# Kernel optimization log

Measured on AMD Instinct MI355X. Metric: run time of the kernel, lower is better.

## Reference

```python
import jax, jax.numpy as jnp
import numpy as np

HEADS = 12
DIM = 768
DH = DIM // HEADS


def setup_inputs() -> dict:
    key = jax.random.key(0)
    k1, k2 = jax.random.split(key)
    z = jax.random.normal(k1, (4, 2048, DIM), dtype=jnp.float32)
    # nn.Linear(dim, 3*dim, bias=False): weight shape [3*dim, dim], y = z @ W.T
    W_qkv = jax.random.normal(k2, (3 * DIM, DIM), dtype=jnp.float32) * (1.0 / np.sqrt(DIM))
    return {"z": z, "W_qkv": W_qkv}


def reference(z, W_qkv):
    b, n, d = z.shape
    qkv = jnp.einsum('bnd,ed->bne', z, W_qkv)  # [b, n, 3*dim]
    # last dim layout is (headNum, m, Dh) per the einops pattern '(headNum m Dh)'
    qkv = qkv.reshape(b, n, HEADS, 3, DH)
    q = jnp.transpose(qkv[:, :, :, 0, :], (0, 2, 1, 3))  # [b, h, n, Dh]
    k = jnp.transpose(qkv[:, :, :, 1, :], (0, 2, 1, 3))
    v = jnp.transpose(qkv[:, :, :, 2, :], (0, 2, 1, 3))
    scores = jnp.einsum('bhqd,bhkd->bhqk', q, k) / np.sqrt(DH).astype(np.float32)
    A = jax.nn.softmax(scores, axis=-1)  # full [b, h, n, n] matrix, as in source
    out = jnp.einsum('bhqk,bhkd->bhqd', A, v)  # [b, h, n, Dh]
    return jnp.transpose(out, (0, 2, 1, 3)).reshape(b, n, d)
```

## Files before the change

### kernel.cpp

```cpp
#include <hip/hip_runtime.h>
#include <hip/hip_bf16.h>
#include <stdint.h>


typedef __attribute__((ext_vector_type(8))) short bf8_t;
typedef __attribute__((ext_vector_type(4))) float f4_t;

__device__ __forceinline__ unsigned short f2bf(float f) {
  union { float f; unsigned u; } x; x.f = f;
  return (unsigned short)((x.u + 0x7fffu + ((x.u >> 16) & 1u)) >> 16);
}
__device__ __forceinline__ unsigned cvt_pk_bf16(float lo, float hi) {
  unsigned r;
  asm("v_cvt_pk_bf16_f32 %0, %1, %2" : "=v"(r) : "v"(lo), "v"(hi));
  return r;
}
__device__ __forceinline__ void gload_lds16(const void* g, void* l) {
  __builtin_amdgcn_global_load_lds(
      (const __attribute__((address_space(1))) void*)g,
      (__attribute__((address_space(3))) void*)l, 16, 0, 0);
}

__global__ __launch_bounds__(256) void cvt_kernel(
    const float* __restrict__ Z, const float* __restrict__ W,
    unsigned short* __restrict__ Zb)
{
  const int idx = blockIdx.x * 256 + threadIdx.x;
  const float* src;
  unsigned short* dst;
  int c;
  if (idx < 786432) { src = Z; dst = Zb; c = idx; }
  else              { src = W; dst = Zb + 6291456; c = idx - 786432; }
  const float4 a0 = *(const float4*)(src + (size_t)c * 8);
  const float4 a1 = *(const float4*)(src + (size_t)c * 8 + 4);
  uint4 pk = { cvt_pk_bf16(a0.x, a0.y), cvt_pk_bf16(a0.z, a0.w),
               cvt_pk_bf16(a1.x, a1.y), cvt_pk_bf16(a1.z, a1.w) };
  *(uint4*)(dst + (size_t)c * 8) = pk;
}

__global__ __launch_bounds__(256, 3) void qkv_gemm_kernel(
    const unsigned short* __restrict__ Zb, const unsigned short* __restrict__ Wb,
    unsigned short* __restrict__ qb, unsigned short* __restrict__ kb,
    unsigned short* __restrict__ vt)
{
  __shared__ __align__(16) unsigned short As[128 * 64];
  __shared__ __align__(16) unsigned short Bs[128 * 64];

  const int tid = threadIdx.x;
  const int w    = tid >> 6;
  const int lane = tid & 63;
  const int g    = lane >> 4;
  const int l15  = lane & 15;
  const int bid0 = blockIdx.y * 18 + blockIdx.x;
  const int bid  = (bid0 & 7) * 144 + (bid0 >> 3);
  const int m0 = (bid / 18) * 128;
  const int n0 = (bid % 18) * 128;
  const int wr = w >> 1, wc = w & 1;

  const int arow = w * 32 + (lane >> 3);
  const int achk = ((lane & 7) ^ (lane >> 3)) * 8;
  const unsigned short* za = Zb + (size_t)(m0 + arow) * 768 + achk;
  const unsigned short* wa = Wb + (size_t)(n0 + arow) * 768 + achk;
  unsigned short* const lza = As + w * 32 * 64;
  unsigned short* const lwa = Bs + w * 32 * 64;

  const f4_t zf = {0.f, 0.f, 0.f, 0.f};
  f4_t acc[4][4];
#pragma unroll
  for (int m = 0; m < 4; ++m)
#pragma unroll
    for (int n = 0; n < 4; ++n) acc[m][n] = zf;

  for (int ks = 0; ks < 12; ++ks) {
    __syncthreads();
#pragma unroll
    for (int r = 0; r < 4; ++r) {
      gload_lds16(za + r * 8 * 768, lza + r * 512);
      gload_lds16(wa + r * 8 * 768, lwa + r * 512);
    }
    za += 64; wa += 64;
    __syncthreads();

#pragma unroll
    for (int s = 0; s < 2; ++s) {
      bf8_t af[4], bfr[4];
#pragma unroll
      for (int m = 0; m < 4; ++m) {
        const int row = wr * 64 + m * 16 + l15;
        af[m] = *(const bf8_t*)(As + row * 64 + (((s * 4 + g) ^ (row & 7)) * 8));
      }
#pragma unroll
      for (int n = 0; n < 4; ++n) {
        const int row = wc * 64 + n * 16 + l15;
        bfr[n] = *(const bf8_t*)(Bs + row * 64 + (((s * 4 + g) ^ (row & 7)) * 8));
      }
      __builtin_amdgcn_s_setprio(1);
#pragma unroll
      for (int m = 0; m < 4; ++m)
#pragma unroll
        for (int n = 0; n < 4; ++n)
          acc[m][n] = __builtin_amdgcn_mfma_f32_16x16x32_bf16(af[m], bfr[n], acc[m][n], 0, 0, 0);
      __builtin_amdgcn_s_setprio(0);
    }
  }

  const float QSCALE = 0.18033688011112042f;
#pragma unroll
  for (int m = 0; m < 4; ++m) {
    const int gi  = m0 + wr * 64 + m * 16 + g * 4;
    const int b   = gi >> 11;
    const int tok = gi & 2047;
#pragma unroll
    for (int n = 0; n < 4; ++n) {
      const int e0  = n0 + wc * 64 + n * 16;
      const int h   = e0 / 192;
      const int rem = e0 - h * 192;
      const int mm  = rem >> 6;
      const int dh  = (rem & 63) + l15;
      if (mm == 2) {
        uint2 pk = { cvt_pk_bf16(acc[m][n][0], acc[m][n][1]),
                     cvt_pk_bf16(acc[m][n][2], acc[m][n][3]) };
        const int pos = ((tok >> 5) & 1) * 32 + ((tok >> 2) & 3) * 8
                      + ((tok >> 4) & 1) * 4;
        const size_t vaddr = ((size_t)(b * 12 + h) * 32 + (tok >> 6)) * 4096
                           + dh * 64 + pos;
        *(uint2*)(vt + vaddr) = pk;
      } else {
        unsigned short* buf = mm ? kb : qb;
        const float sc = mm ? 1.0f : QSCALE;
        const size_t base = ((size_t)((b * 12 + h) * 2048 + tok)) * 64 + dh;
#pragma unroll
        for (int j = 0; j < 4; ++j)
          buf[base + (size_t)j * 64] = f2bf(acc[m][n][j] * sc);
      }
    }
  }
}

__global__ __launch_bounds__(256, 3) void attn_kernel(
    const unsigned short* __restrict__ qb, const unsigned short* __restrict__ kb,
    const unsigned short* __restrict__ vt, float* __restrict__ out)
{
  __shared__ __align__(16) unsigned short Ks[2][64 * 64];
  __shared__ __align__(16) unsigned short Vs[2][64 * 64];

  const int bid = blockIdx.x;
  const int nb  = (bid & 7) * 96 + (bid >> 3);
  const int bh  = nb >> 4;
  const int qt  = nb & 15;
  const int tid = threadIdx.x;
  const int w    = tid >> 6;
  const int lane = tid & 63;
  const int g    = lane >> 4;
  const int l15  = lane & 15;

  const unsigned short* Qh  = qb + (size_t)bh * 2048 * 64;
  const unsigned short* Kh  = kb + (size_t)bh * 2048 * 64;
  const unsigned short* VTh = vt + (size_t)bh * 32 * 4096;

  const int qbase = qt * 128 + w * 32;

  bf8_t qfr[2][2];
#pragma unroll
  for (int qq = 0; qq < 2; ++qq)
#pragma unroll
    for (int s = 0; s < 2; ++s)
      qfr[qq][s] = *(const bf8_t*)(Qh + (size_t)(qbase + qq * 16 + l15) * 64 + s * 32 + g * 8);

  const int xk   = l15 & 7;
  const int offA = l15 * 64 + ((g) ^ xk) * 8;
  const int offB = l15 * 64 + ((4 + g) ^ xk) * 8;

  const size_t dmaoff = (size_t)(w * 16 + (lane >> 3)) * 64
                      + ((lane & 7) ^ (lane >> 3)) * 8;
  const unsigned short* ksrc = Kh + dmaoff;
  const unsigned short* vsrc = VTh + dmaoff;
  const int ldsoff = w * 16 * 64;

  gload_lds16(ksrc,                 &Ks[0][ldsoff]);
  gload_lds16(ksrc + 8 * 64,        &Ks[0][ldsoff + 8 * 64]);
  gload_lds16(vsrc,                 &Vs[0][ldsoff]);
  gload_lds16(vsrc + 8 * 64,        &Vs[0][ldsoff + 8 * 64]);
  gload_lds16(ksrc + 4096,          &Ks[1][ldsoff]);
  gload_lds16(ksrc + 4096 + 8 * 64, &Ks[1][ldsoff + 8 * 64]);
  gload_lds16(vsrc + 4096,          &Vs[1][ldsoff]);
  gload_lds16(vsrc + 4096 + 8 * 64, &Vs[1][ldsoff + 8 * 64]);
  __syncthreads();

  const unsigned short* kdma = ksrc + 2 * 4096;
  const unsigned short* vdma = vsrc + 2 * 4096;

  const f4_t m16 = {-16.f, -16.f, -16.f, -16.f};
  const f4_t zf  = {0.f, 0.f, 0.f, 0.f};
  f4_t accO[2][4];
  float lsumP[2] = {0.f, 0.f};
#pragma unroll
  for (int qq = 0; qq < 2; ++qq)
#pragma unroll
    for (int nf = 0; nf < 4; ++nf) accO[qq][nf] = zf;

  for (int t = 0; t < 32; ++t) {
    const int cur = t & 1;
    const unsigned short* pK = &Ks[cur][0];
    const unsigned short* pV = &Vs[cur][0];

    bf8_t ka[4][2];
#pragma unroll
    for (int kf = 0; kf < 4; ++kf) {
      ka[kf][0] = *(const bf8_t*)(pK + offA + kf * 1024);
      ka[kf][1] = *(const bf8_t*)(pK + offB + kf * 1024);
    }
    bf8_t vfr[2][4];
#pragma unroll
    for (int nf = 0; nf < 4; ++nf) {
      vfr[0][nf] = *(const bf8_t*)(pV + offA + nf * 1024);
      vfr[1][nf] = *(const bf8_t*)(pV + offB + nf * 1024);
    }

    __syncthreads();

    if (t < 30) {
      gload_lds16(kdma,          &Ks[cur][ldsoff]);
      gload_lds16(kdma + 8 * 64, &Ks[cur][ldsoff + 8 * 64]);
      gload_lds16(vdma,          &Vs[cur][ldsoff]);
      gload_lds16(vdma + 8 * 64, &Vs[cur][ldsoff + 8 * 64]);
      kdma += 4096; vdma += 4096;
    }

    f4_t accS0[4], accS1[4];
    __builtin_amdgcn_s_setprio(1);
#pragma unroll
    for (int kf = 0; kf < 4; ++kf) {
      f4_t a = __builtin_amdgcn_mfma_f32_16x16x32_bf16(ka[kf][0], qfr[0][0], m16, 0, 0, 0);
      accS0[kf] = __builtin_amdgcn_mfma_f32_16x16x32_bf16(ka[kf][1], qfr[0][1], a, 0, 0, 0);
    }
#pragma unroll
    for (int kf = 0; kf < 4; ++kf) {
      f4_t a = __builtin_amdgcn_mfma_f32_16x16x32_bf16(ka[kf][0], qfr[1][0], m16, 0, 0, 0);
      accS1[kf] = __builtin_amdgcn_mfma_f32_16x16x32_bf16(ka[kf][1], qfr[1][1], a, 0, 0, 0);
    }
    __builtin_amdgcn_s_setprio(0);

#pragma unroll
    for (int qq = 0; qq < 2; ++qq) {
      const f4_t* accS = qq ? accS1 : accS0;
      union { bf8_t v[2]; unsigned uw[8]; } P8;
      float ps = 0.f;
#pragma unroll
      for (int kf = 0; kf < 4; ++kf) {
        const float p0 = __builtin_amdgcn_exp2f(accS[kf][0]);
        const float p1 = __builtin_amdgcn_exp2f(accS[kf][1]);
        const float p2 = __builtin_amdgcn_exp2f(accS[kf][2]);
        const float p3 = __builtin_amdgcn_exp2f(accS[kf][3]);
        ps += (p0 + p1) + (p2 + p3);
        P8.uw[kf * 2]     = cvt_pk_bf16(p0, p1);
        P8.uw[kf * 2 + 1] = cvt_pk_bf16(p2, p3);
      }
      lsumP[qq] += ps;

      __builtin_amdgcn_s_setprio(1);
#pragma unroll
      for (int kk = 0; kk < 2; ++kk)
#pragma unroll
        for (int nf = 0; nf < 4; ++nf)
          accO[qq][nf] = __builtin_amdgcn_mfma_f32_16x16x32_bf16(P8.v[kk], vfr[kk][nf], accO[qq][nf], 0, 0, 0);
      __builtin_amdgcn_s_setprio(0);
    }
  }

  const int b = bh / 12, h = bh - (bh / 12) * 12;
#pragma unroll
  for (int qq = 0; qq < 2; ++qq) {
    float ls = lsumP[qq];
    ls += __shfl_xor(ls, 16);
    ls += __shfl_xor(ls, 32);
    const float rl = 1.0f / ls;
    f4_t lv;
#pragma unroll
    for (int j = 0; j < 4; ++j) lv[j] = __shfl(rl, g * 4 + j);
#pragma unroll
    for (int nf = 0; nf < 4; ++nf) {
#pragma unroll
      for (int j = 0; j < 4; ++j) {
        const int qrow = qbase + qq * 16 + g * 4 + j;
        out[((size_t)(b * 2048 + qrow)) * 768 + h * 64 + nf * 16 + l15] = accO[qq][nf][j] * lv[j];
      }
    }
  }
}

extern "C" void kernel_launch(void* const* d_in, const int* in_sizes, int n_in,
                              void* d_out, int out_size, void* d_ws, size_t ws_size,
                              hipStream_t stream) {
  (void)in_sizes; (void)n_in; (void)out_size; (void)ws_size;
  const float* Z = (const float*)d_in[0];
  const float* W = (const float*)d_in[1];
  float* out = (float*)d_out;

  unsigned short* qb = (unsigned short*)d_ws;
  unsigned short* kb = qb + (size_t)48 * 2048 * 64;
  unsigned short* vt = kb + (size_t)48 * 2048 * 64;

  unsigned short* Zb = (unsigned short*)d_out;
  unsigned short* Wb = Zb + (size_t)8192 * 768;

  cvt_kernel<<<dim3(3936), 256, 0, stream>>>(Z, W, Zb);
  qkv_gemm_kernel<<<dim3(18, 64), 256, 0, stream>>>(Zb, Wb, qb, kb, vt);
  attn_kernel<<<dim3(768), 256, 0, stream>>>(qb, kb, vt, out);
}
```

Before: 105.2 us.

## Use two waves per attention block, each handling 64 query rows

The attention kernel now runs with 128 threads (two waves) per block instead of four, and each wave processes 64 query rows (four 16-row groups) instead of 32. Each wave reuses the K and V fragments it loaded from LDS across more MFMAs, and each thread issues twice as many DMA loads. The cost is more accumulator registers per thread and fewer waves per workgroup to hide latency. Launch bounds change to (128,2), which may reduce occupancy.

```diff
diff --git a/kernel.cpp b/kernel.cpp
--- a/kernel.cpp
+++ b/kernel.cpp
@@ -137,7 +137,7 @@
   }
 }
 
-__global__ __launch_bounds__(256, 3) void attn_kernel(
+__global__ __launch_bounds__(128, 2) void attn_kernel(
     const unsigned short* __restrict__ qb, const unsigned short* __restrict__ kb,
     const unsigned short* __restrict__ vt, float* __restrict__ out)
 {
@@ -158,11 +158,11 @@
   const unsigned short* Kh  = kb + (size_t)bh * 2048 * 64;
   const unsigned short* VTh = vt + (size_t)bh * 32 * 4096;
 
-  const int qbase = qt * 128 + w * 32;
-
-  bf8_t qfr[2][2];
-#pragma unroll
-  for (int qq = 0; qq < 2; ++qq)
+  const int qbase = qt * 128 + w * 64;
+
+  bf8_t qfr[4][2];
+#pragma unroll
+  for (int qq = 0; qq < 4; ++qq)
 #pragma unroll
     for (int s = 0; s < 2; ++s)
       qfr[qq][s] = *(const bf8_t*)(Qh + (size_t)(qbase + qq * 16 + l15) * 64 + s * 32 + g * 8);
@@ -171,20 +171,19 @@
   const int offA = l15 * 64 + ((g) ^ xk) * 8;
   const int offB = l15 * 64 + ((4 + g) ^ xk) * 8;
 
-  const size_t dmaoff = (size_t)(w * 16 + (lane >> 3)) * 64
+  const size_t dmaoff = (size_t)(w * 32 + (lane >> 3)) * 64
                       + ((lane & 7) ^ (lane >> 3)) * 8;
   const unsigned short* ksrc = Kh + dmaoff;
   const unsigned short* vsrc = VTh + dmaoff;
-  const int ldsoff = w * 16 * 64;
-
-  gload_lds16(ksrc,                 &Ks[0][ldsoff]);
-  gload_lds16(ksrc + 8 * 64,        &Ks[0][ldsoff + 8 * 64]);
-  gload_lds16(vsrc,                 &Vs[0][ldsoff]);
-  gload_lds16(vsrc + 8 * 64,        &Vs[0][ldsoff + 8 * 64]);
-  gload_lds16(ksrc + 4096,          &Ks[1][ldsoff]);
-  gload_lds16(ksrc + 4096 + 8 * 64, &Ks[1][ldsoff + 8 * 64]);
-  gload_lds16(vsrc + 4096,          &Vs[1][ldsoff]);
-  gload_lds16(vsrc + 4096 + 8 * 64, &Vs[1][ldsoff + 8 * 64]);
+  const int ldsoff = w * 32 * 64;
+
+#pragma unroll
+  for (int r = 0; r < 4; ++r) {
+    gload_lds16(ksrc + r * 8 * 64,        &Ks[0][ldsoff + r * 512]);
+    gload_lds16(vsrc + r * 8 * 64,        &Vs[0][ldsoff + r * 512]);
+    gload_lds16(ksrc + 4096 + r * 8 * 64, &Ks[1][ldsoff + r * 512]);
+    gload_lds16(vsrc + 4096 + r * 8 * 64, &Vs[1][ldsoff + r * 512]);
+  }
   __syncthreads();
 
   const unsigned short* kdma = ksrc + 2 * 4096;
@@ -192,10 +191,10 @@
 
   const f4_t m16 = {-16.f, -16.f, -16.f, -16.f};
   const f4_t zf  = {0.f, 0.f, 0.f, 0.f};
-  f4_t accO[2][4];
-  float lsumP[2] = {0.f, 0.f};
-#pragma unroll
-  for (int qq = 0; qq < 2; ++qq)
+  f4_t accO[4][4];
+  float lsumP[4] = {0.f, 0.f, 0.f, 0.f};
+#pragma unroll
+  for (int qq = 0; qq < 4; ++qq)
 #pragma unroll
     for (int nf = 0; nf < 4; ++nf) accO[qq][nf] = zf;
 
@@ -220,57 +219,62 @@
     __syncthreads();
 
     if (t < 30) {
-      gload_lds16(kdma,          &Ks[cur][ldsoff]);
-      gload_lds16(kdma + 8 * 64, &Ks[cur][ldsoff + 8 * 64]);
-      gload_lds16(vdma,          &Vs[cur][ldsoff]);
-      gload_lds16(vdma + 8 * 64, &Vs[cur][ldsoff + 8 * 64]);
+#pragma unroll
+      for (int r = 0; r < 4; ++r) {
+        gload_lds16(kdma + r * 8 * 64, &Ks[cur][ldsoff + r * 512]);
+        gload_lds16(vdma + r * 8 * 64, &Vs[cur][ldsoff + r * 512]);
+      }
       kdma += 4096; vdma += 4096;
     }
 
-    f4_t accS0[4], accS1[4];
-    __builtin_amdgcn_s_setprio(1);
-#pragma unroll
-    for (int kf = 0; kf < 4; ++kf) {
-      f4_t a = __builtin_amdgcn_mfma_f32_16x16x32_bf16(ka[kf][0], qfr[0][0], m16, 0, 0, 0);
-      accS0[kf] = __builtin_amdgcn_mfma_f32_16x16x32_bf16(ka[kf][1], qfr[0][1], a, 0, 0, 0);
-    }
-#pragma unroll
-    for (int kf = 0; kf < 4; ++kf) {
-      f4_t a = __builtin_amdgcn_mfma_f32_16x16x32_bf16(ka[kf][0], qfr[1][0], m16, 0, 0, 0);
-      accS1[kf] = __builtin_amdgcn_mfma_f32_16x16x32_bf16(ka[kf][1], qfr[1][1], a, 0, 0, 0);
-    }
-    __builtin_amdgcn_s_setprio(0);
-
-#pragma unroll
-    for (int qq = 0; qq < 2; ++qq) {
-      const f4_t* accS = qq ? accS1 : accS0;
-      union { bf8_t v[2]; unsigned uw[8]; } P8;
-      float ps = 0.f;
+#pragma unroll
+    for (int qp = 0; qp < 2; ++qp) {
+      f4_t accSa[4], accSb[4];
+      __builtin_amdgcn_s_setprio(1);
 #pragma unroll
       for (int kf = 0; kf < 4; ++kf) {
-        const float p0 = __builtin_amdgcn_exp2f(accS[kf][0]);
-        const float p1 = __builtin_amdgcn_exp2f(accS[kf][1]);
-        const float p2 = __builtin_amdgcn_exp2f(accS[kf][2]);
-        const float p3 = __builtin_amdgcn_exp2f(accS[kf][3]);
-        ps += (p0 + p1) + (p2 + p3);
-        P8.uw[kf * 2]     = cvt_pk_bf16(p0, p1);
-        P8.uw[kf * 2 + 1] = cvt_pk_bf16(p2, p3);
-      }
-      lsumP[qq] += ps;
-
-      __builtin_amdgcn_s_setprio(1);
-#pragma unroll
-      for (int kk = 0; kk < 2; ++kk)
-#pragma unroll
-        for (int nf = 0; nf < 4; ++nf)
-          accO[qq][nf] = __builtin_amdgcn_mfma_f32_16x16x32_bf16(P8.v[kk], vfr[kk][nf], accO[qq][nf], 0, 0, 0);
+        f4_t a = __builtin_amdgcn_mfma_f32_16x16x32_bf16(ka[kf][0], qfr[qp * 2][0], m16, 0, 0, 0);
+        accSa[kf] = __builtin_amdgcn_mfma_f32_16x16x32_bf16(ka[kf][1], qfr[qp * 2][1], a, 0, 0, 0);
+      }
+#pragma unroll
+      for (int kf = 0; kf < 4; ++kf) {
+        f4_t a = __builtin_amdgcn_mfma_f32_16x16x32_bf16(ka[kf][0], qfr[qp * 2 + 1][0], m16, 0, 0, 0);
+        accSb[kf] = __builtin_amdgcn_mfma_f32_16x16x32_bf16(ka[kf][1], qfr[qp * 2 + 1][1], a, 0, 0, 0);
+      }
       __builtin_amdgcn_s_setprio(0);
+
+#pragma unroll
+      for (int qh = 0; qh < 2; ++qh) {
+        const int qq = qp * 2 + qh;
+        const f4_t* accS = qh ? accSb : accSa;
+        union { bf8_t v[2]; unsigned uw[8]; } P8;
+        float ps = 0.f;
+#pragma unroll
+        for (int kf = 0; kf < 4; ++kf) {
+          const float p0 = __builtin_amdgcn_exp2f(accS[kf][0]);
+          const float p1 = __builtin_amdgcn_exp2f(accS[kf][1]);
+          const float p2 = __builtin_amdgcn_exp2f(accS[kf][2]);
+          const float p3 = __builtin_amdgcn_exp2f(accS[kf][3]);
+          ps += (p0 + p1) + (p2 + p3);
+          P8.uw[kf * 2]     = cvt_pk_bf16(p0, p1);
+          P8.uw[kf * 2 + 1] = cvt_pk_bf16(p2, p3);
+        }
+        lsumP[qq] += ps;
+
+        __builtin_amdgcn_s_setprio(1);
+#pragma unroll
+        for (int kk = 0; kk < 2; ++kk)
+#pragma unroll
+          for (int nf = 0; nf < 4; ++nf)
+            accO[qq][nf] = __builtin_amdgcn_mfma_f32_16x16x32_bf16(P8.v[kk], vfr[kk][nf], accO[qq][nf], 0, 0, 0);
+        __builtin_amdgcn_s_setprio(0);
+      }
     }
   }
 
   const int b = bh / 12, h = bh - (bh / 12) * 12;
 #pragma unroll
-  for (int qq = 0; qq < 2; ++qq) {
+  for (int qq = 0; qq < 4; ++qq) {
     float ls = lsumP[qq];
     ls += __shfl_xor(ls, 16);
     ls += __shfl_xor(ls, 32);
@@ -306,5 +310,5 @@
 
   cvt_kernel<<<dim3(3936), 256, 0, stream>>>(Z, W, Zb);
   qkv_gemm_kernel<<<dim3(18, 64), 256, 0, stream>>>(Zb, Wb, qb, kb, vt);
-  attn_kernel<<<dim3(768), 256, 0, stream>>>(qb, kb, vt, out);
-}
+  attn_kernel<<<dim3(768), 128, 0, stream>>>(qb, kb, vt, out);
+}
```

Result: slower. 116.5 us (+10.7%).

## Split attention KV range across two blocks and combine partial results

Applied to the files above, without the earlier changes.

Splits the key/value sequence into two halves so the attention kernel launches twice as many blocks, each handling 16 KV tiles. Each block writes unnormalized partial outputs and row sums, and a new combine kernel adds the two partials and normalizes. The aim is more blocks per CU and better occupancy on a grid that was only 768 blocks. The cost is extra global traffic for the second partial buffer and an additional kernel launch. The split path depends on the workspace being large enough and falls back to the old single-block path otherwise.

```diff
diff --git a/kernel.cpp b/kernel.cpp
--- a/kernel.cpp
+++ b/kernel.cpp
@@ -137,17 +137,29 @@
   }
 }
 
-__global__ __launch_bounds__(256, 3) void attn_kernel(
+template <int SPLIT>
+__global__ __launch_bounds__(256, 3) void attn_body(
     const unsigned short* __restrict__ qb, const unsigned short* __restrict__ kb,
-    const unsigned short* __restrict__ vt, float* __restrict__ out)
+    const unsigned short* __restrict__ vt, float* __restrict__ out0,
+    float* __restrict__ out1, float* __restrict__ lsb)
 {
   __shared__ __align__(16) unsigned short Ks[2][64 * 64];
   __shared__ __align__(16) unsigned short Vs[2][64 * 64];
 
+  const int NT = SPLIT ? 16 : 32;
   const int bid = blockIdx.x;
-  const int nb  = (bid & 7) * 96 + (bid >> 3);
-  const int bh  = nb >> 4;
-  const int qt  = nb & 15;
+  int bh, qt, half;
+  if (SPLIT) {
+    const int nb = (bid & 7) * 192 + (bid >> 3);
+    qt = nb & 15;
+    half = (nb >> 4) & 1;
+    bh = nb >> 5;
+  } else {
+    const int nb = (bid & 7) * 96 + (bid >> 3);
+    qt = nb & 15;
+    half = 0;
+    bh = nb >> 4;
+  }
   const int tid = threadIdx.x;
   const int w    = tid >> 6;
   const int lane = tid & 63;
@@ -155,8 +167,8 @@
   const int l15  = lane & 15;
 
   const unsigned short* Qh  = qb + (size_t)bh * 2048 * 64;
-  const unsigned short* Kh  = kb + (size_t)bh * 2048 * 64;
-  const unsigned short* VTh = vt + (size_t)bh * 32 * 4096;
+  const unsigned short* Kh  = kb + (size_t)bh * 2048 * 64 + (size_t)half * 16 * 4096;
+  const unsigned short* VTh = vt + (size_t)bh * 32 * 4096 + (size_t)half * 16 * 4096;
 
   const int qbase = qt * 128 + w * 32;
 
@@ -199,7 +211,7 @@
 #pragma unroll
     for (int nf = 0; nf < 4; ++nf) accO[qq][nf] = zf;
 
-  for (int t = 0; t < 32; ++t) {
+  for (int t = 0; t < NT; ++t) {
     const int cur = t & 1;
     const unsigned short* pK = &Ks[cur][0];
     const unsigned short* pV = &Vs[cur][0];
@@ -219,7 +231,7 @@
 
     __syncthreads();
 
-    if (t < 30) {
+    if (t < NT - 2) {
       gload_lds16(kdma,          &Ks[cur][ldsoff]);
       gload_lds16(kdma + 8 * 64, &Ks[cur][ldsoff + 8 * 64]);
       gload_lds16(vdma,          &Vs[cur][ldsoff]);
@@ -269,30 +281,69 @@
   }
 
   const int b = bh / 12, h = bh - (bh / 12) * 12;
+  float* const outP = (SPLIT && half) ? out1 : out0;
 #pragma unroll
   for (int qq = 0; qq < 2; ++qq) {
     float ls = lsumP[qq];
     ls += __shfl_xor(ls, 16);
     ls += __shfl_xor(ls, 32);
-    const float rl = 1.0f / ls;
-    f4_t lv;
-#pragma unroll
-    for (int j = 0; j < 4; ++j) lv[j] = __shfl(rl, g * 4 + j);
-#pragma unroll
-    for (int nf = 0; nf < 4; ++nf) {
-#pragma unroll
-      for (int j = 0; j < 4; ++j) {
-        const int qrow = qbase + qq * 16 + g * 4 + j;
-        out[((size_t)(b * 2048 + qrow)) * 768 + h * 64 + nf * 16 + l15] = accO[qq][nf][j] * lv[j];
-      }
-    }
-  }
+    if (SPLIT) {
+      if (g == 0)
+        lsb[((size_t)half * 48 + bh) * 2048 + qbase + qq * 16 + l15] = ls;
+#pragma unroll
+      for (int nf = 0; nf < 4; ++nf)
+#pragma unroll
+        for (int j = 0; j < 4; ++j) {
+          const int qrow = qbase + qq * 16 + g * 4 + j;
+          outP[((size_t)(b * 2048 + qrow)) * 768 + h * 64 + nf * 16 + l15] = accO[qq][nf][j];
+        }
+    } else {
+      const float rl = 1.0f / ls;
+      f4_t lv;
+#pragma unroll
+      for (int j = 0; j < 4; ++j) lv[j] = __shfl(rl, g * 4 + j);
+#pragma unroll
+      for (int nf = 0; nf < 4; ++nf)
+#pragma unroll
+        for (int j = 0; j < 4; ++j) {
+          const int qrow = qbase + qq * 16 + g * 4 + j;
+          outP[((size_t)(b * 2048 + qrow)) * 768 + h * 64 + nf * 16 + l15] = accO[qq][nf][j] * lv[j];
+        }
+    }
+  }
+}
+
+__global__ __launch_bounds__(256) void combine_kernel(
+    float* __restrict__ out, const float* __restrict__ P1,
+    const float* __restrict__ lsb)
+{
+  const int tid = blockIdx.x * 256 + threadIdx.x;
+  const int row = tid >> 3;
+  const int dh0 = (tid & 7) * 8;
+  const int bh  = row >> 11;
+  const int tok = row & 2047;
+  const int b   = bh / 12, h = bh - (bh / 12) * 12;
+
+  const float ls = lsb[row] + lsb[(size_t)48 * 2048 + row];
+  const float rl = 1.0f / ls;
+
+  const size_t base = ((size_t)(b * 2048 + tok)) * 768 + h * 64 + dh0;
+  float4 a0 = *(const float4*)(out + base);
+  float4 a1 = *(const float4*)(out + base + 4);
+  const float4 b0 = *(const float4*)(P1 + base);
+  const float4 b1 = *(const float4*)(P1 + base + 4);
+  a0.x = (a0.x + b0.x) * rl; a0.y = (a0.y + b0.y) * rl;
+  a0.z = (a0.z + b0.z) * rl; a0.w = (a0.w + b0.w) * rl;
+  a1.x = (a1.x + b1.x) * rl; a1.y = (a1.y + b1.y) * rl;
+  a1.z = (a1.z + b1.z) * rl; a1.w = (a1.w + b1.w) * rl;
+  *(float4*)(out + base)     = a0;
+  *(float4*)(out + base + 4) = a1;
 }
 
 extern "C" void kernel_launch(void* const* d_in, const int* in_sizes, int n_in,
                               void* d_out, int out_size, void* d_ws, size_t ws_size,
                               hipStream_t stream) {
-  (void)in_sizes; (void)n_in; (void)out_size; (void)ws_size;
+  (void)in_sizes; (void)n_in; (void)out_size;
   const float* Z = (const float*)d_in[0];
   const float* W = (const float*)d_in[1];
   float* out = (float*)d_out;
@@ -301,10 +352,22 @@
   unsigned short* kb = qb + (size_t)48 * 2048 * 64;
   unsigned short* vt = kb + (size_t)48 * 2048 * 64;
 
+  float* P1  = (float*)(vt + (size_t)48 * 32 * 4096);
+  float* lsb = P1 + (size_t)48 * 2048 * 64;
+  const size_t WS_NEEDED = ((size_t)48 * 2048 * 64 * 2) * 3
+                         + (size_t)48 * 2048 * 64 * 4
+                         + (size_t)2 * 48 * 2048 * 4;
+
   unsigned short* Zb = (unsigned short*)d_out;
   unsigned short* Wb = Zb + (size_t)8192 * 768;
 
   cvt_kernel<<<dim3(3936), 256, 0, stream>>>(Z, W, Zb);
   qkv_gemm_kernel<<<dim3(18, 64), 256, 0, stream>>>(Zb, Wb, qb, kb, vt);
-  attn_kernel<<<dim3(768), 256, 0, stream>>>(qb, kb, vt, out);
-}
+
+  if (ws_size >= WS_NEEDED) {
+    attn_body<1><<<dim3(1536), 256, 0, stream>>>(qb, kb, vt, out, P1, lsb);
+    combine_kernel<<<dim3(3072), 256, 0, stream>>>(out, P1, lsb);
+  } else {
+    attn_body<0><<<dim3(768), 256, 0, stream>>>(qb, kb, vt, out, nullptr, nullptr);
+  }
+}
```

Result: slower. 118.4 us, median of 2 (+12.5%).
